# Performance work log

Measured on AMD Instinct MI355X. Metric: run time of the kernel, lower is better.

The kernel has to match this reference:

```python
import jax, jax.numpy as jnp
import numpy as np

H, W, C = 64, 64, 64
B = 64
N_HEADS = 4
CONV_FILTERS = 64
BASIS_DIM = 16


def get_spatial_basis(h, w, d):
    half_d = d // 2
    basis = np.zeros((h, w, d), dtype=np.float32)
    div = np.exp(np.arange(0, half_d, 2, dtype=np.float32) * -np.log(100.0) / half_d)
    h_grid = np.expand_dims(np.arange(0, h, dtype=np.float32), 1)
    w_grid = np.expand_dims(np.arange(0, w, dtype=np.float32), 1)
    basis[:, :, 0:half_d:2] = np.sin(h_grid * div)[:, np.newaxis, :]
    basis[:, :, 1:half_d:2] = np.cos(h_grid * div)[:, np.newaxis, :]
    basis[:, :, half_d::2] = np.sin(w_grid * div)[np.newaxis, :, :]
    basis[:, :, half_d + 1::2] = np.cos(w_grid * div)[np.newaxis, :, :]
    return basis


def setup_inputs() -> dict:
    key = jax.random.key(0)
    ks = jax.random.split(key, 8)
    feat_in = C + BASIS_DIM  # 80 input channels for 1x1 convs
    return {
        "image": jax.random.normal(ks[0], (B, H, W, C), jnp.float32),
        "state1": jax.random.normal(ks[1], (B, 512), jnp.float32),
        "state2": jax.random.normal(ks[2], (B, 512), jnp.float32),
        "extra": jax.random.normal(ks[3], (B, 256), jnp.float32),
        "Wq": jax.random.normal(ks[4], (1024, CONV_FILTERS), jnp.float32) * 0.03,
        "bq": jnp.zeros((CONV_FILTERS,), jnp.float32),
        "Wk": jax.random.normal(ks[5], (feat_in, CONV_FILTERS), jnp.float32) * 0.1,
        "bk": jnp.zeros((CONV_FILTERS,), jnp.float32),
        "Wv": jax.random.normal(ks[6], (feat_in, CONV_FILTERS), jnp.float32) * 0.1,
        "bv": jnp.zeros((CONV_FILTERS,), jnp.float32),
        "spatial_basis": jnp.asarray(get_spatial_basis(H, W, BASIS_DIM)),
    }


def reference(image, state1, state2, extra, Wq, bq, Wk, bk, Wv, bv, spatial_basis):
    b, h, w, _ = image.shape
    nh = N_HEADS
    cf = Wq.shape[1]
    dph = cf // nh  # depth per head

    # concat image with tiled spatial basis -> [B,h,w,C+basis_dim]
    sb = jnp.broadcast_to(spatial_basis[None], (b,) + spatial_basis.shape)
    feats = jnp.concatenate([image, sb], axis=-1)

    # combiner over network-state tensors, then Dense query
    state = jnp.concatenate([state1, state2], axis=-1)  # [B,1024]
    q = state @ Wq + bq                                 # [B,cf]

    # 1x1 convs == per-pixel dense projections
    keys = feats @ Wk + bk    # [B,h,w,cf]
    vals = feats @ Wv + bv    # [B,h,w,cf]

    qh = q.reshape(b, nh, dph)
    kh = keys.reshape(b, h * w, nh, dph)
    vh = vals.reshape(b, h * w, nh, dph)

    # per-head dot scores over spatial positions, softmax over positions
    scores = jnp.einsum('bnd,bpnd->bpn', qh, kh)        # [B,hw,nh]
    attn = jax.nn.softmax(scores, axis=1)
    mean_attn = attn.mean(axis=-1).reshape(b, h, w)

    # weighted sum of values over spatial positions -> [B,cf]
    pooled = jnp.einsum('bpn,bpnd->bnd', attn, vh).reshape(b, cf)

    out = jnp.concatenate([pooled, extra], axis=-1)
    return out, mean_attn
```

## Files before the change

### kernel.cpp

```cpp
#include <hip/hip_runtime.h>
#include <hip/hip_bf16.h>

#define BATCH  64
#define HW     4096
#define PTILE  256
#define NSPLIT 16
#define RST    264

typedef unsigned int u32;
typedef unsigned short u16;

__device__ __forceinline__ float bf2f(u16 h) { return __uint_as_float(((u32)h) << 16); }

__device__ __forceinline__ u32 f2bf(float x) {
  u32 b = __float_as_uint(x);
  return (b + 0x7fffu + ((b >> 16) & 1u)) >> 16;
}

template<bool F32>
__device__ __forceinline__ float ld(const void* p, size_t i) {
  if (F32) return ((const float*)p)[i];
  return bf2f(((const u16*)p)[i]);
}

template<bool F32>
__device__ __forceinline__ float4 ld4(const void* p, size_t i4) {
  if (F32) return ((const float4*)p)[i4];
  uint2 u = ((const uint2*)p)[i4];
  return make_float4(bf2f(u.x & 0xffff), bf2f(u.x >> 16), bf2f(u.y & 0xffff), bf2f(u.y >> 16));
}

template<bool F32>
__device__ __forceinline__ void st(void* p, size_t i, float v) {
  if (F32) ((float*)p)[i] = v;
  else     ((__hip_bfloat16*)p)[i] = __float2bfloat16(v);
}

__device__ __forceinline__ bool detect_f32(const u16* __restrict__ image) {
  u16 h = image[(threadIdx.x & 63) * 2];
  u32 e = (h >> 7) & 0xFFu;
  unsigned long long m = __ballot(e >= 0x86u);
  return __popcll(m) >= 8;
}

template<bool F32>
__device__ void k1a_body(const void* state1, const void* state2, const void* Wq,
                         float* q_part, float* WslT, float* stt) {
  const int kb = blockIdx.x;
  const int tid = threadIdx.x;
#pragma unroll
  for (int i = 0; i < 4; ++i) {
    const int fidx = i * 256 + tid;
    const int r = fidx >> 4, c4 = fidx & 15;
    float4 v = ld4<F32>(Wq, (size_t)(kb * 64 + r) * 16 + c4);
    WslT[(c4 * 4 + 0) * 68 + r] = v.x;
    WslT[(c4 * 4 + 1) * 68 + r] = v.y;
    WslT[(c4 * 4 + 2) * 68 + r] = v.z;
    WslT[(c4 * 4 + 3) * 68 + r] = v.w;
  }
  const void* src = (kb < 8) ? state1 : state2;
  const int k0q = (kb & 7) * 16;
#pragma unroll
  for (int i = 0; i < 4; ++i) {
    const int fidx = i * 256 + tid;
    const int bb = fidx >> 4, i4 = fidx & 15;
    float4 v = ld4<F32>(src, (size_t)bb * 128 + k0q + i4);
    *(float4*)&stt[bb * 64 + i4 * 4] = v;
  }
  __syncthreads();
  const int j = tid & 63, bg = tid >> 6;
  float acc[16];
#pragma unroll
  for (int b2 = 0; b2 < 16; ++b2) acc[b2] = 0.f;
#pragma unroll
  for (int i4 = 0; i4 < 16; ++i4) {
    float4 wv = *(const float4*)&WslT[j * 68 + i4 * 4];
#pragma unroll
    for (int b2 = 0; b2 < 16; ++b2) {
      float4 sv = *(const float4*)&stt[(bg * 16 + b2) * 64 + i4 * 4];
      acc[b2] += wv.x * sv.x + wv.y * sv.y + wv.z * sv.z + wv.w * sv.w;
    }
  }
#pragma unroll
  for (int b2 = 0; b2 < 16; ++b2)
    q_part[kb * 4096 + (bg * 16 + b2) * 64 + j] = acc[b2];
}

__global__ __launch_bounds__(256) void k1a(
    const void* image, const void* state1, const void* state2, const void* Wq, float* q_part) {
  __shared__ float WslT[64 * 68];
  __shared__ float stt[64 * 64];
  if (detect_f32((const u16*)image)) k1a_body<true >(state1, state2, Wq, q_part, WslT, stt);
  else                               k1a_body<false>(state1, state2, Wq, q_part, WslT, stt);
}

template<bool F32>
__device__ void k1b_body(const float* q_part, const void* bq, const void* Wk, const void* bk,
                         float* weff, float* cb, float* q) {
  const int b = blockIdx.x, tid = threadIdx.x;
  if (tid < 64) {
    float a = ld<F32>(bq, tid);
#pragma unroll
    for (int sl = 0; sl < 16; ++sl) a += q_part[sl * 4096 + b * 64 + tid];
    q[tid] = a;
  }
  __syncthreads();
  if (tid < 320) {
    const int c = tid >> 2, n = tid & 3;
    float a = 0.f;
#pragma unroll
    for (int d = 0; d < 16; ++d) a += ld<F32>(Wk, (size_t)c * 64 + n * 16 + d) * q[n * 16 + d];
    weff[b * 320 + tid] = a;
  }
  if (tid >= 256 && tid < 260) {
    const int n = tid - 256;
    float a = 0.f;
#pragma unroll
    for (int d = 0; d < 16; ++d) a += ld<F32>(bk, n * 16 + d) * q[n * 16 + d];
    cb[b * 4 + n] = a;
  }
}

__global__ __launch_bounds__(320) void k1b(
    const void* image, const float* q_part, const void* bq, const void* Wk, const void* bk,
    float* weff, float* cb) {
  __shared__ float q[64];
  if (detect_f32((const u16*)image)) k1b_body<true >(q_part, bq, Wk, bk, weff, cb, q);
  else                               k1b_body<false>(q_part, bq, Wk, bk, weff, cb, q);
}

__global__ __launch_bounds__(256) void k2_main(
    const void* __restrict__ image, const void* __restrict__ basis,
    const float* __restrict__ weff, const float* __restrict__ cb,
    float* __restrict__ e_buf, float* __restrict__ m_blk, float* __restrict__ sum_blk,
    float* __restrict__ fpool_part) {
  __shared__ __align__(16) u16 featT[80 * RST];
  __shared__ __align__(16) float es_t[4 * PTILE];
  __shared__ float weffL[320];
  __shared__ float cbL[4];
  __shared__ float red[16], red2[16], bm[4];
  const int tid = threadIdx.x;
  const int b = blockIdx.x & 63, s = blockIdx.x >> 6;
  const int bs = b * NSPLIT + s;

  for (int i = tid; i < 320; i += 256) weffL[i] = weff[b * 320 + i];
  if (tid < 4) cbL[tid] = cb[b * 4 + tid];

  if (detect_f32((const u16*)image)) {
    const float4* img4 = (const float4*)image + ((size_t)(b * HW + s * PTILE)) * 16;
#pragma unroll
    for (int i = 0; i < 8; ++i) {
      const int fidx = i * 256 + tid;
      const int pp = fidx >> 4, c4 = fidx & 15;
      float4 v0 = img4[(pp * 2) * 16 + c4];
      float4 v1 = img4[(pp * 2 + 1) * 16 + c4];
      *(u32*)&featT[(c4 * 4 + 0) * RST + pp * 2] = f2bf(v0.x) | (f2bf(v1.x) << 16);
      *(u32*)&featT[(c4 * 4 + 1) * RST + pp * 2] = f2bf(v0.y) | (f2bf(v1.y) << 16);
      *(u32*)&featT[(c4 * 4 + 2) * RST + pp * 2] = f2bf(v0.z) | (f2bf(v1.z) << 16);
      *(u32*)&featT[(c4 * 4 + 3) * RST + pp * 2] = f2bf(v0.w) | (f2bf(v1.w) << 16);
    }
    const float4* bas4 = (const float4*)basis + (size_t)(s * PTILE) * 4;
#pragma unroll
    for (int i = 0; i < 2; ++i) {
      const int fidx = i * 256 + tid;
      const int pp = fidx >> 2, c4 = fidx & 3;
      float4 v0 = bas4[(pp * 2) * 4 + c4];
      float4 v1 = bas4[(pp * 2 + 1) * 4 + c4];
      *(u32*)&featT[(64 + c4 * 4 + 0) * RST + pp * 2] = f2bf(v0.x) | (f2bf(v1.x) << 16);
      *(u32*)&featT[(64 + c4 * 4 + 1) * RST + pp * 2] = f2bf(v0.y) | (f2bf(v1.y) << 16);
      *(u32*)&featT[(64 + c4 * 4 + 2) * RST + pp * 2] = f2bf(v0.z) | (f2bf(v1.z) << 16);
      *(u32*)&featT[(64 + c4 * 4 + 3) * RST + pp * 2] = f2bf(v0.w) | (f2bf(v1.w) << 16);
    }
  } else {
    const uint4* img4 = (const uint4*)image + ((size_t)(b * HW + s * PTILE)) * 8;
#pragma unroll
    for (int i = 0; i < 4; ++i) {
      const int fidx = i * 256 + tid;
      const int pp = fidx >> 3, c8 = fidx & 7;
      uint4 u0 = img4[(pp * 2) * 8 + c8];
      uint4 u1 = img4[(pp * 2 + 1) * 8 + c8];
      const u32 w0[4] = {u0.x, u0.y, u0.z, u0.w};
      const u32 w1[4] = {u1.x, u1.y, u1.z, u1.w};
#pragma unroll
      for (int h = 0; h < 4; ++h) {
        *(u32*)&featT[(c8 * 8 + 2 * h + 0) * RST + pp * 2] = (w0[h] & 0xffffu) | (w1[h] << 16);
        *(u32*)&featT[(c8 * 8 + 2 * h + 1) * RST + pp * 2] = (w0[h] >> 16) | (w1[h] & 0xffff0000u);
      }
    }
    const uint4* bas4 = (const uint4*)basis + (size_t)(s * PTILE) * 2;
    {
      const int pp = tid >> 1, h8 = tid & 1;
      uint4 u0 = bas4[(pp * 2) * 2 + h8];
      uint4 u1 = bas4[(pp * 2 + 1) * 2 + h8];
      const u32 w0[4] = {u0.x, u0.y, u0.z, u0.w};
      const u32 w1[4] = {u1.x, u1.y, u1.z, u1.w};
#pragma unroll
      for (int h = 0; h < 4; ++h) {
        *(u32*)&featT[(64 + h8 * 8 + 2 * h + 0) * RST + pp * 2] = (w0[h] & 0xffffu) | (w1[h] << 16);
        *(u32*)&featT[(64 + h8 * 8 + 2 * h + 1) * RST + pp * 2] = (w0[h] >> 16) | (w1[h] & 0xffff0000u);
      }
    }
  }
  __syncthreads();

  const int p8 = tid >> 3, cg = tid & 7;
  float acc[8][4];
#pragma unroll
  for (int pp = 0; pp < 8; ++pp)
#pragma unroll
    for (int n = 0; n < 4; ++n) acc[pp][n] = (cg == 0) ? cbL[n] : 0.f;
#pragma unroll
  for (int ci = 0; ci < 10; ++ci) {
    const int c = cg + 8 * ci;
    uint4 fv = *(const uint4*)&featT[c * RST + ((tid >> 3) & 7) * 8 + (tid >> 6) * 64];
    fv = *(const uint4*)&featT[c * RST + p8 * 8];
    float4 wv = *(const float4*)&weffL[c * 4];
    const u32 uu[4] = {fv.x, fv.y, fv.z, fv.w};
#pragma unroll
    for (int i = 0; i < 4; ++i) {
      float lo = __uint_as_float(uu[i] << 16);
      float hi = __uint_as_float(uu[i] & 0xffff0000u);
      acc[2 * i][0] += lo * wv.x; acc[2 * i][1] += lo * wv.y;
      acc[2 * i][2] += lo * wv.z; acc[2 * i][3] += lo * wv.w;
      acc[2 * i + 1][0] += hi * wv.x; acc[2 * i + 1][1] += hi * wv.y;
      acc[2 * i + 1][2] += hi * wv.z; acc[2 * i + 1][3] += hi * wv.w;
    }
  }
#pragma unroll
  for (int off = 1; off <= 4; off <<= 1)
#pragma unroll
    for (int pp = 0; pp < 8; ++pp)
#pragma unroll
      for (int n = 0; n < 4; ++n) acc[pp][n] += __shfl_xor(acc[pp][n], off, 64);

  float mx[4];
#pragma unroll
  for (int n = 0; n < 4; ++n) {
    float m = acc[0][n];
#pragma unroll
    for (int pp = 1; pp < 8; ++pp) m = fmaxf(m, acc[pp][n]);
    mx[n] = m;
  }
#pragma unroll
  for (int off = 8; off <= 32; off <<= 1)
#pragma unroll
    for (int n = 0; n < 4; ++n) mx[n] = fmaxf(mx[n], __shfl_xor(mx[n], off, 64));
  if ((tid & 63) == 0) {
    float* r = red + (tid >> 6) * 4;
    r[0] = mx[0]; r[1] = mx[1]; r[2] = mx[2]; r[3] = mx[3];
  }
  __syncthreads();
  if (tid < 4) {
    float m = red[tid];
#pragma unroll
    for (int w = 1; w < 4; ++w) m = fmaxf(m, red[w * 4 + tid]);
    bm[tid] = m;
  }
  __syncthreads();

#pragma unroll
  for (int pp = 0; pp < 8; ++pp)
#pragma unroll
    for (int n = 0; n < 4; ++n) acc[pp][n] = __expf(acc[pp][n] - bm[n]);

  if (cg == 0) {
#pragma unroll
    for (int n = 0; n < 4; ++n) {
      float4 eA = make_float4(acc[0][n], acc[1][n], acc[2][n], acc[3][n]);
      float4 eB = make_float4(acc[4][n], acc[5][n], acc[6][n], acc[7][n]);
      *(float4*)&es_t[n * PTILE + p8 * 8]     = eA;
      *(float4*)&es_t[n * PTILE + p8 * 8 + 4] = eB;
      float4* ebp = (float4*)e_buf + (size_t)(b * 4 + n) * 1024 + s * 64 + p8 * 2;
      ebp[0] = eA; ebp[1] = eB;
    }
  }
  float sm[4];
#pragma unroll
  for (int n = 0; n < 4; ++n) {
    float a = acc[0][n];
#pragma unroll
    for (int pp = 1; pp < 8; ++pp) a += acc[pp][n];
    sm[n] = a;
  }
#pragma unroll
  for (int off = 8; off <= 32; off <<= 1)
#pragma unroll
    for (int n = 0; n < 4; ++n) sm[n] += __shfl_xor(sm[n], off, 64);
  if ((tid & 63) == 0) {
    float* r = red2 + (tid >> 6) * 4;
    r[0] = sm[0]; r[1] = sm[1]; r[2] = sm[2]; r[3] = sm[3];
  }
  __syncthreads();
  if (tid < 4) {
    float a = red2[tid] + red2[4 + tid] + red2[8 + tid] + red2[12 + tid];
    sum_blk[bs * 4 + tid] = a;
    m_blk[bs * 4 + tid] = bm[tid];
  }

  {
    const int n = tid >> 6, c = tid & 63;
    const float4* esn = (const float4*)(es_t + n * PTILE);
    float a1 = 0.f, a2 = 0.f;
#pragma unroll 4
    for (int g = 0; g < 32; ++g) {
      float4 ex = esn[g * 2], ey = esn[g * 2 + 1];
      uint4 fv = *(const uint4*)&featT[c * RST + g * 8];
      const u32 uu[4] = {fv.x, fv.y, fv.z, fv.w};
      a1 += ex.x * __uint_as_float(uu[0] << 16) + ex.y * __uint_as_float(uu[0] & 0xffff0000u)
          + ex.z * __uint_as_float(uu[1] << 16) + ex.w * __uint_as_float(uu[1] & 0xffff0000u)
          + ey.x * __uint_as_float(uu[2] << 16) + ey.y * __uint_as_float(uu[2] & 0xffff0000u)
          + ey.z * __uint_as_float(uu[3] << 16) + ey.w * __uint_as_float(uu[3] & 0xffff0000u);
      if (c < 16) {
        uint4 f2 = *(const uint4*)&featT[(64 + c) * RST + g * 8];
        const u32 vv[4] = {f2.x, f2.y, f2.z, f2.w};
        a2 += ex.x * __uint_as_float(vv[0] << 16) + ex.y * __uint_as_float(vv[0] & 0xffff0000u)
            + ex.z * __uint_as_float(vv[1] << 16) + ex.w * __uint_as_float(vv[1] & 0xffff0000u)
            + ey.x * __uint_as_float(vv[2] << 16) + ey.y * __uint_as_float(vv[2] & 0xffff0000u)
            + ey.z * __uint_as_float(vv[3] << 16) + ey.w * __uint_as_float(vv[3] & 0xffff0000u);
      }
    }
    fpool_part[(size_t)bs * 320 + n * 80 + c] = a1;
    if (c < 16) fpool_part[(size_t)bs * 320 + n * 80 + 64 + c] = a2;
  }
}

template<bool F32>
__device__ void k34_body(const float* m_blk, const float* sum_blk, const float* e_buf,
                         const float* fpool_part, const void* Wv, const void* bv,
                         const void* extra, void* out, float* esc, float* fp) {
  const int tid = threadIdx.x;
  const int b = blockIdx.x & 63, s = blockIdx.x >> 6;
  if (tid < 4) {
    float M = -3.4e38f;
#pragma unroll
    for (int sp = 0; sp < NSPLIT; ++sp) M = fmaxf(M, m_blk[(b * NSPLIT + sp) * 4 + tid]);
    float den = 0.f;
#pragma unroll
    for (int sp = 0; sp < NSPLIT; ++sp)
      den += __expf(m_blk[(b * NSPLIT + sp) * 4 + tid] - M) * sum_blk[(b * NSPLIT + sp) * 4 + tid];
    float rd = 1.0f / den;
#pragma unroll
    for (int sp = 0; sp < NSPLIT; ++sp)
      esc[sp * 4 + tid] = __expf(m_blk[(b * NSPLIT + sp) * 4 + tid] - M) * rd;
  }
  __syncthreads();
  {
    const size_t pidx = (size_t)s * PTILE + tid;
    float e0 = e_buf[(size_t)(b * 4 + 0) * HW + pidx];
    float e1 = e_buf[(size_t)(b * 4 + 1) * HW + pidx];
    float e2 = e_buf[(size_t)(b * 4 + 2) * HW + pidx];
    float e3 = e_buf[(size_t)(b * 4 + 3) * HW + pidx];
    float mean = 0.25f * (e0 * esc[s * 4 + 0] + e1 * esc[s * 4 + 1] +
                          e2 * esc[s * 4 + 2] + e3 * esc[s * 4 + 3]);
    st<F32>(out, (size_t)BATCH * 320 + (size_t)b * HW + pidx, mean);
  }
  if (s == 0) {
    for (int idx = tid; idx < 320; idx += 256) {
      const int n2 = idx / 80;
      float a = 0.f;
#pragma unroll
      for (int sp = 0; sp < NSPLIT; ++sp)
        a += esc[sp * 4 + n2] * fpool_part[(size_t)(b * NSPLIT + sp) * 320 + idx];
      fp[idx] = a;
    }
    __syncthreads();
    if (tid < 64) {
      const int n = tid >> 4;
      float dot = 0.f;
#pragma unroll
      for (int c = 0; c < 80; ++c) dot += fp[n * 80 + c] * ld<F32>(Wv, (size_t)c * 64 + tid);
      st<F32>(out, (size_t)b * 320 + tid, dot + ld<F32>(bv, tid));
    }
    st<F32>(out, (size_t)b * 320 + 64 + tid, ld<F32>(extra, (size_t)b * 256 + tid));
  }
}

__global__ __launch_bounds__(256) void k34_out(
    const void* image, const float* m_blk, const float* sum_blk, const float* e_buf,
    const float* fpool_part, const void* Wv, const void* bv, const void* extra, void* out) {
  __shared__ float esc[NSPLIT * 4];
  __shared__ float fp[320];
  if (detect_f32((const u16*)image))
       k34_body<true >(m_blk, sum_blk, e_buf, fpool_part, Wv, bv, extra, out, esc, fp);
  else k34_body<false>(m_blk, sum_blk, e_buf, fpool_part, Wv, bv, extra, out, esc, fp);
}

extern "C" void kernel_launch(void* const* d_in, const int* in_sizes, int n_in,
                              void* d_out, int out_size, void* d_ws, size_t ws_size,
                              hipStream_t stream) {
  (void)in_sizes; (void)n_in; (void)out_size; (void)ws_size;
  const void* image  = d_in[0];
  const void* state1 = d_in[1];
  const void* state2 = d_in[2];
  const void* extra  = d_in[3];
  const void* Wq = d_in[4];
  const void* bq = d_in[5];
  const void* Wk = d_in[6];
  const void* bk = d_in[7];
  const void* Wv = d_in[8];
  const void* bv = d_in[9];
  const void* basis = d_in[10];

  float* ws         = (float*)d_ws;
  float* weff       = ws;
  float* cb         = ws + 20480;
  float* m_blk      = ws + 20736;
  float* sum_blk    = ws + 24832;
  float* q_part     = ws + 28928;
  float* fpool_part = ws + 94464;
  float* e_buf      = ws + 422144;

  k1a<<<dim3(16), dim3(256), 0, stream>>>(image, state1, state2, Wq, q_part);
  k1b<<<dim3(BATCH), dim3(320), 0, stream>>>(image, q_part, bq, Wk, bk, weff, cb);
  k2_main<<<dim3(BATCH * NSPLIT), dim3(PTILE), 0, stream>>>(image, basis, weff, cb,
                                                            e_buf, m_blk, sum_blk, fpool_part);
  k34_out<<<dim3(BATCH * NSPLIT), dim3(PTILE), 0, stream>>>(image, m_blk, sum_blk, e_buf,
                                                            fpool_part, Wv, bv, extra, d_out);
}
```

Measured before the change: 142.7 us.

## Use bf16 MFMA for score and pooling GEMMs with smaller pixel tiles

Replaces the scalar FMA score computation and the weighted feature pooling in the main kernel with 16x16x32 bf16 MFMA instructions. To feed them, features are staged in shared memory in both row-major and transposed layouts, and the effective key weights are stored as padded bf16. The pixel tile shrinks from 256 to 128, so there are 32 splits per batch, and the exp buffer is stored as bf16 to halve its traffic. The trade-off is lower precision on the exponentials, more shared-memory staging, and a larger partial-reduction workload in the output kernel.

Result: faster. 131.5 us (-7.8%).

```diff
diff --git a/kernel.cpp b/kernel.cpp
--- a/kernel.cpp
+++ b/kernel.cpp
@@ -1,35 +1,36 @@
 #include <hip/hip_runtime.h>
 #include <hip/hip_bf16.h>
 
-#define BATCH  64
-#define HW     4096
-#define PTILE  256
-#define NSPLIT 16
-#define RST    264
+#define BATCH 64
+#define HW    4096
+#define PT    128
+#define NS    32
+#define FR_ST 104
+#define FT_ST 136
 
 typedef unsigned int u32;
 typedef unsigned short u16;
+typedef __attribute__((ext_vector_type(8))) short bf16x8;
+typedef __attribute__((ext_vector_type(4))) float f32x4;
 
 __device__ __forceinline__ float bf2f(u16 h) { return __uint_as_float(((u32)h) << 16); }
-
 __device__ __forceinline__ u32 f2bf(float x) {
   u32 b = __float_as_uint(x);
   return (b + 0x7fffu + ((b >> 16) & 1u)) >> 16;
 }
+__device__ __forceinline__ u32 pkbf(float lo, float hi) { return f2bf(lo) | (f2bf(hi) << 16); }
 
 template<bool F32>
 __device__ __forceinline__ float ld(const void* p, size_t i) {
   if (F32) return ((const float*)p)[i];
   return bf2f(((const u16*)p)[i]);
 }
-
 template<bool F32>
 __device__ __forceinline__ float4 ld4(const void* p, size_t i4) {
   if (F32) return ((const float4*)p)[i4];
   uint2 u = ((const uint2*)p)[i4];
   return make_float4(bf2f(u.x & 0xffff), bf2f(u.x >> 16), bf2f(u.y & 0xffff), bf2f(u.y >> 16));
 }
-
 template<bool F32>
 __device__ __forceinline__ void st(void* p, size_t i, float v) {
   if (F32) ((float*)p)[i] = v;
@@ -96,8 +97,10 @@
 
 template<bool F32>
 __device__ void k1b_body(const float* q_part, const void* bq, const void* Wk, const void* bk,
-                         float* weff, float* cb, float* q) {
+                         u16* weffbt, float* cb, float* q) {
   const int b = blockIdx.x, tid = threadIdx.x;
+  u32* wz = (u32*)(weffbt + (size_t)b * 1664);
+  for (int i = tid; i < 832; i += 320) wz[i] = 0u;
   if (tid < 64) {
     float a = ld<F32>(bq, tid);
 #pragma unroll
@@ -110,7 +113,7 @@
     float a = 0.f;
 #pragma unroll
     for (int d = 0; d < 16; ++d) a += ld<F32>(Wk, (size_t)c * 64 + n * 16 + d) * q[n * 16 + d];
-    weff[b * 320 + tid] = a;
+    weffbt[(size_t)b * 1664 + n * 104 + c] = (u16)f2bf(a);
   }
   if (tid >= 256 && tid < 260) {
     const int n = tid - 256;
@@ -123,244 +126,231 @@
 
 __global__ __launch_bounds__(320) void k1b(
     const void* image, const float* q_part, const void* bq, const void* Wk, const void* bk,
-    float* weff, float* cb) {
+    u16* weffbt, float* cb) {
   __shared__ float q[64];
-  if (detect_f32((const u16*)image)) k1b_body<true >(q_part, bq, Wk, bk, weff, cb, q);
-  else                               k1b_body<false>(q_part, bq, Wk, bk, weff, cb, q);
+  if (detect_f32((const u16*)image)) k1b_body<true >(q_part, bq, Wk, bk, weffbt, cb, q);
+  else                               k1b_body<false>(q_part, bq, Wk, bk, weffbt, cb, q);
 }
 
 __global__ __launch_bounds__(256) void k2_main(
     const void* __restrict__ image, const void* __restrict__ basis,
-    const float* __restrict__ weff, const float* __restrict__ cb,
-    float* __restrict__ e_buf, float* __restrict__ m_blk, float* __restrict__ sum_blk,
+    const float* __restrict__ cb, const u16* __restrict__ weffbt,
+    u16* __restrict__ e_buf, float* __restrict__ m_blk, float* __restrict__ sum_blk,
     float* __restrict__ fpool_part) {
-  __shared__ __align__(16) u16 featT[80 * RST];
-  __shared__ __align__(16) float es_t[4 * PTILE];
-  __shared__ float weffL[320];
-  __shared__ float cbL[4];
-  __shared__ float red[16], red2[16], bm[4];
+  __shared__ __align__(16) u16 smem[25936];
+  float* redf  = (float*)(smem + 25856);
+  float* red2f = (float*)(smem + 25888);
+  float* bmf   = (float*)(smem + 25920);
+  float* cbL   = (float*)(smem + 25928);
+
   const int tid = threadIdx.x;
   const int b = blockIdx.x & 63, s = blockIdx.x >> 6;
-  const int bs = b * NSPLIT + s;
-
-  for (int i = tid; i < 320; i += 256) weffL[i] = weff[b * 320 + i];
-  if (tid < 4) cbL[tid] = cb[b * 4 + tid];
+  const int bs = b * NS + s;
+  const int wave = tid >> 6, lane = tid & 63;
+  const int m = lane & 15, q = lane >> 4;
 
   if (detect_f32((const u16*)image)) {
-    const float4* img4 = (const float4*)image + ((size_t)(b * HW + s * PTILE)) * 16;
-#pragma unroll
-    for (int i = 0; i < 8; ++i) {
-      const int fidx = i * 256 + tid;
-      const int pp = fidx >> 4, c4 = fidx & 15;
-      float4 v0 = img4[(pp * 2) * 16 + c4];
-      float4 v1 = img4[(pp * 2 + 1) * 16 + c4];
-      *(u32*)&featT[(c4 * 4 + 0) * RST + pp * 2] = f2bf(v0.x) | (f2bf(v1.x) << 16);
-      *(u32*)&featT[(c4 * 4 + 1) * RST + pp * 2] = f2bf(v0.y) | (f2bf(v1.y) << 16);
-      *(u32*)&featT[(c4 * 4 + 2) * RST + pp * 2] = f2bf(v0.z) | (f2bf(v1.z) << 16);
-      *(u32*)&featT[(c4 * 4 + 3) * RST + pp * 2] = f2bf(v0.w) | (f2bf(v1.w) << 16);
-    }
-    const float4* bas4 = (const float4*)basis + (size_t)(s * PTILE) * 4;
-#pragma unroll
-    for (int i = 0; i < 2; ++i) {
-      const int fidx = i * 256 + tid;
-      const int pp = fidx >> 2, c4 = fidx & 3;
-      float4 v0 = bas4[(pp * 2) * 4 + c4];
-      float4 v1 = bas4[(pp * 2 + 1) * 4 + c4];
-      *(u32*)&featT[(64 + c4 * 4 + 0) * RST + pp * 2] = f2bf(v0.x) | (f2bf(v1.x) << 16);
-      *(u32*)&featT[(64 + c4 * 4 + 1) * RST + pp * 2] = f2bf(v0.y) | (f2bf(v1.y) << 16);
-      *(u32*)&featT[(64 + c4 * 4 + 2) * RST + pp * 2] = f2bf(v0.z) | (f2bf(v1.z) << 16);
-      *(u32*)&featT[(64 + c4 * 4 + 3) * RST + pp * 2] = f2bf(v0.w) | (f2bf(v1.w) << 16);
-    }
-  } else {
-    const uint4* img4 = (const uint4*)image + ((size_t)(b * HW + s * PTILE)) * 8;
+    const float4* img4 = (const float4*)image + ((size_t)(b * HW + s * PT)) * 16;
 #pragma unroll
     for (int i = 0; i < 4; ++i) {
       const int fidx = i * 256 + tid;
-      const int pp = fidx >> 3, c8 = fidx & 7;
-      uint4 u0 = img4[(pp * 2) * 8 + c8];
-      uint4 u1 = img4[(pp * 2 + 1) * 8 + c8];
+      const int pq = fidx >> 4, c4 = fidx & 15;
+      float4 v0 = img4[(pq * 2) * 16 + c4];
+      float4 v1 = img4[(pq * 2 + 1) * 16 + c4];
+      *(uint2*)&smem[(pq * 2) * FR_ST + c4 * 4]     = make_uint2(pkbf(v0.x, v0.y), pkbf(v0.z, v0.w));
+      *(uint2*)&smem[(pq * 2 + 1) * FR_ST + c4 * 4] = make_uint2(pkbf(v1.x, v1.y), pkbf(v1.z, v1.w));
+      const float a0[4] = {v0.x, v0.y, v0.z, v0.w};
+      const float a1[4] = {v1.x, v1.y, v1.z, v1.w};
+#pragma unroll
+      for (int k = 0; k < 4; ++k)
+        *(u32*)&smem[13312 + (c4 * 4 + k) * FT_ST + pq * 2] = pkbf(a0[k], a1[k]);
+    }
+    const float4* bas4 = (const float4*)basis + (size_t)(s * PT) * 4;
+    {
+      const int pq = tid >> 2, c4 = tid & 3;
+      float4 v0 = bas4[(pq * 2) * 4 + c4];
+      float4 v1 = bas4[(pq * 2 + 1) * 4 + c4];
+      *(uint2*)&smem[(pq * 2) * FR_ST + 64 + c4 * 4]     = make_uint2(pkbf(v0.x, v0.y), pkbf(v0.z, v0.w));
+      *(uint2*)&smem[(pq * 2 + 1) * FR_ST + 64 + c4 * 4] = make_uint2(pkbf(v1.x, v1.y), pkbf(v1.z, v1.w));
+      const float a0[4] = {v0.x, v0.y, v0.z, v0.w};
+      const float a1[4] = {v1.x, v1.y, v1.z, v1.w};
+#pragma unroll
+      for (int k = 0; k < 4; ++k)
+        *(u32*)&smem[13312 + (64 + c4 * 4 + k) * FT_ST + pq * 2] = pkbf(a0[k], a1[k]);
+    }
+  } else {
+    const uint4* img4 = (const uint4*)image + ((size_t)(b * HW + s * PT)) * 4;
+    {
+      const int pq = tid >> 2, c8 = tid & 3;
+      uint4 u0 = img4[(pq * 2) * 4 + c8];
+      uint4 u1 = img4[(pq * 2 + 1) * 4 + c8];
+      *(uint4*)&smem[(pq * 2) * FR_ST + c8 * 8]     = u0;
+      *(uint4*)&smem[(pq * 2 + 1) * FR_ST + c8 * 8] = u1;
       const u32 w0[4] = {u0.x, u0.y, u0.z, u0.w};
       const u32 w1[4] = {u1.x, u1.y, u1.z, u1.w};
 #pragma unroll
-      for (int h = 0; h < 4; ++h) {
-        *(u32*)&featT[(c8 * 8 + 2 * h + 0) * RST + pp * 2] = (w0[h] & 0xffffu) | (w1[h] << 16);
-        *(u32*)&featT[(c8 * 8 + 2 * h + 1) * RST + pp * 2] = (w0[h] >> 16) | (w1[h] & 0xffff0000u);
+      for (int k = 0; k < 4; ++k) {
+        *(u32*)&smem[13312 + (c8 * 8 + 2 * k) * FT_ST + pq * 2]     = (w0[k] & 0xffffu) | (w1[k] << 16);
+        *(u32*)&smem[13312 + (c8 * 8 + 2 * k + 1) * FT_ST + pq * 2] = (w0[k] >> 16) | (w1[k] & 0xffff0000u);
       }
     }
-    const uint4* bas4 = (const uint4*)basis + (size_t)(s * PTILE) * 2;
-    {
-      const int pp = tid >> 1, h8 = tid & 1;
-      uint4 u0 = bas4[(pp * 2) * 2 + h8];
-      uint4 u1 = bas4[(pp * 2 + 1) * 2 + h8];
+    const uint4* bas4 = (const uint4*)basis + (size_t)(s * PT) * 2;
+    if (tid < 128) {
+      const int pq = tid >> 1, c8 = tid & 1;
+      uint4 u0 = bas4[(pq * 2) * 2 + c8];
+      uint4 u1 = bas4[(pq * 2 + 1) * 2 + c8];
+      *(uint4*)&smem[(pq * 2) * FR_ST + 64 + c8 * 8]     = u0;
+      *(uint4*)&smem[(pq * 2 + 1) * FR_ST + 64 + c8 * 8] = u1;
       const u32 w0[4] = {u0.x, u0.y, u0.z, u0.w};
       const u32 w1[4] = {u1.x, u1.y, u1.z, u1.w};
 #pragma unroll
-      for (int h = 0; h < 4; ++h) {
-        *(u32*)&featT[(64 + h8 * 8 + 2 * h + 0) * RST + pp * 2] = (w0[h] & 0xffffu) | (w1[h] << 16);
-        *(u32*)&featT[(64 + h8 * 8 + 2 * h + 1) * RST + pp * 2] = (w0[h] >> 16) | (w1[h] & 0xffff0000u);
+      for (int k = 0; k < 4; ++k) {
+        *(u32*)&smem[13312 + (64 + c8 * 8 + 2 * k) * FT_ST + pq * 2]     = (w0[k] & 0xffffu) | (w1[k] << 16);
+        *(u32*)&smem[13312 + (64 + c8 * 8 + 2 * k + 1) * FT_ST + pq * 2] = (w0[k] >> 16) | (w1[k] & 0xffff0000u);
       }
     }
   }
-  __syncthreads();
-
-  const int p8 = tid >> 3, cg = tid & 7;
-  float acc[8][4];
-#pragma unroll
-  for (int pp = 0; pp < 8; ++pp)
-#pragma unroll
-    for (int n = 0; n < 4; ++n) acc[pp][n] = (cg == 0) ? cbL[n] : 0.f;
-#pragma unroll
-  for (int ci = 0; ci < 10; ++ci) {
-    const int c = cg + 8 * ci;
-    uint4 fv = *(const uint4*)&featT[c * RST + ((tid >> 3) & 7) * 8 + (tid >> 6) * 64];
-    fv = *(const uint4*)&featT[c * RST + p8 * 8];
-    float4 wv = *(const float4*)&weffL[c * 4];
-    const u32 uu[4] = {fv.x, fv.y, fv.z, fv.w};
-#pragma unroll
-    for (int i = 0; i < 4; ++i) {
-      float lo = __uint_as_float(uu[i] << 16);
-      float hi = __uint_as_float(uu[i] & 0xffff0000u);
-      acc[2 * i][0] += lo * wv.x; acc[2 * i][1] += lo * wv.y;
-      acc[2 * i][2] += lo * wv.z; acc[2 * i][3] += lo * wv.w;
-      acc[2 * i + 1][0] += hi * wv.x; acc[2 * i + 1][1] += hi * wv.y;
-      acc[2 * i + 1][2] += hi * wv.z; acc[2 * i + 1][3] += hi * wv.w;
-    }
-  }
-#pragma unroll
-  for (int off = 1; off <= 4; off <<= 1)
-#pragma unroll
-    for (int pp = 0; pp < 8; ++pp)
-#pragma unroll
-      for (int n = 0; n < 4; ++n) acc[pp][n] += __shfl_xor(acc[pp][n], off, 64);
-
-  float mx[4];
-#pragma unroll
-  for (int n = 0; n < 4; ++n) {
-    float m = acc[0][n];
-#pragma unroll
-    for (int pp = 1; pp < 8; ++pp) m = fmaxf(m, acc[pp][n]);
-    mx[n] = m;
-  }
-#pragma unroll
-  for (int off = 8; off <= 32; off <<= 1)
-#pragma unroll
-    for (int n = 0; n < 4; ++n) mx[n] = fmaxf(mx[n], __shfl_xor(mx[n], off, 64));
-  if ((tid & 63) == 0) {
-    float* r = red + (tid >> 6) * 4;
-    r[0] = mx[0]; r[1] = mx[1]; r[2] = mx[2]; r[3] = mx[3];
+  if (tid < 128) {
+    *(uint4*)&smem[tid * FR_ST + 80] = make_uint4(0, 0, 0, 0);
+    *(uint4*)&smem[tid * FR_ST + 88] = make_uint4(0, 0, 0, 0);
+  }
+  if (tid < 208) {
+    uint4 v = ((const uint4*)(weffbt + (size_t)b * 1664))[tid];
+    *(uint4*)&smem[24192 + tid * 8] = v;
+  }
+  if (tid < 4) cbL[tid] = cb[b * 4 + tid];
+  __syncthreads();
+
+  f32x4 accS[2];
+  {
+    const float ci = (m < 4) ? cbL[m] : 0.f;
+#pragma unroll
+    for (int t = 0; t < 2; ++t) { accS[t][0] = ci; accS[t][1] = ci; accS[t][2] = ci; accS[t][3] = ci; }
+#pragma unroll
+    for (int t = 0; t < 2; ++t) {
+      const int T = wave * 2 + t;
+#pragma unroll
+      for (int s3 = 0; s3 < 3; ++s3) {
+        bf16x8 a = *(const bf16x8*)&smem[(T * 16 + m) * FR_ST + s3 * 32 + q * 8];
+        bf16x8 bb = *(const bf16x8*)&smem[24192 + m * FR_ST + s3 * 32 + q * 8];
+        accS[t] = __builtin_amdgcn_mfma_f32_16x16x32_bf16(a, bb, accS[t], 0, 0, 0);
+      }
+    }
+  }
+  {
+    float mx = accS[0][0];
+#pragma unroll
+    for (int t = 0; t < 2; ++t)
+#pragma unroll
+      for (int r = 0; r < 4; ++r) mx = fmaxf(mx, accS[t][r]);
+    mx = fmaxf(mx, __shfl_xor(mx, 16, 64));
+    mx = fmaxf(mx, __shfl_xor(mx, 32, 64));
+    if (lane < 4) redf[wave * 4 + lane] = mx;
+  }
+  __syncthreads();
+  if (tid < 4)
+    bmf[tid] = fmaxf(fmaxf(redf[tid], redf[4 + tid]), fmaxf(redf[8 + tid], redf[12 + tid]));
+  for (int i = tid; i < 816; i += 256) ((u32*)smem)[272 + i] = 0u;
+  __syncthreads();
+
+  {
+    const float bmv = bmf[m & 3];
+    float ss = 0.f;
+#pragma unroll
+    for (int t = 0; t < 2; ++t) {
+      const int T = wave * 2 + t;
+#pragma unroll
+      for (int r = 0; r < 4; ++r) {
+        float e = __expf(accS[t][r] - bmv);
+        u32 eb = f2bf(e);
+        float er = bf2f((u16)eb);
+        ss += er;
+        if (m < 4) smem[m * FT_ST + T * 16 + q * 4 + r] = (u16)eb;
+      }
+    }
+    ss += __shfl_xor(ss, 16, 64);
+    ss += __shfl_xor(ss, 32, 64);
+    if (lane < 4) red2f[wave * 4 + lane] = ss;
   }
   __syncthreads();
   if (tid < 4) {
-    float m = red[tid];
-#pragma unroll
-    for (int w = 1; w < 4; ++w) m = fmaxf(m, red[w * 4 + tid]);
-    bm[tid] = m;
-  }
-  __syncthreads();
-
-#pragma unroll
-  for (int pp = 0; pp < 8; ++pp)
-#pragma unroll
-    for (int n = 0; n < 4; ++n) acc[pp][n] = __expf(acc[pp][n] - bm[n]);
-
-  if (cg == 0) {
-#pragma unroll
-    for (int n = 0; n < 4; ++n) {
-      float4 eA = make_float4(acc[0][n], acc[1][n], acc[2][n], acc[3][n]);
-      float4 eB = make_float4(acc[4][n], acc[5][n], acc[6][n], acc[7][n]);
-      *(float4*)&es_t[n * PTILE + p8 * 8]     = eA;
-      *(float4*)&es_t[n * PTILE + p8 * 8 + 4] = eB;
-      float4* ebp = (float4*)e_buf + (size_t)(b * 4 + n) * 1024 + s * 64 + p8 * 2;
-      ebp[0] = eA; ebp[1] = eB;
-    }
-  }
-  float sm[4];
-#pragma unroll
-  for (int n = 0; n < 4; ++n) {
-    float a = acc[0][n];
-#pragma unroll
-    for (int pp = 1; pp < 8; ++pp) a += acc[pp][n];
-    sm[n] = a;
-  }
-#pragma unroll
-  for (int off = 8; off <= 32; off <<= 1)
-#pragma unroll
-    for (int n = 0; n < 4; ++n) sm[n] += __shfl_xor(sm[n], off, 64);
-  if ((tid & 63) == 0) {
-    float* r = red2 + (tid >> 6) * 4;
-    r[0] = sm[0]; r[1] = sm[1]; r[2] = sm[2]; r[3] = sm[3];
-  }
-  __syncthreads();
-  if (tid < 4) {
-    float a = red2[tid] + red2[4 + tid] + red2[8 + tid] + red2[12 + tid];
-    sum_blk[bs * 4 + tid] = a;
-    m_blk[bs * 4 + tid] = bm[tid];
-  }
-
-  {
-    const int n = tid >> 6, c = tid & 63;
-    const float4* esn = (const float4*)(es_t + n * PTILE);
-    float a1 = 0.f, a2 = 0.f;
-#pragma unroll 4
-    for (int g = 0; g < 32; ++g) {
-      float4 ex = esn[g * 2], ey = esn[g * 2 + 1];
-      uint4 fv = *(const uint4*)&featT[c * RST + g * 8];
-      const u32 uu[4] = {fv.x, fv.y, fv.z, fv.w};
-      a1 += ex.x * __uint_as_float(uu[0] << 16) + ex.y * __uint_as_float(uu[0] & 0xffff0000u)
-          + ex.z * __uint_as_float(uu[1] << 16) + ex.w * __uint_as_float(uu[1] & 0xffff0000u)
-          + ey.x * __uint_as_float(uu[2] << 16) + ey.y * __uint_as_float(uu[2] & 0xffff0000u)
-          + ey.z * __uint_as_float(uu[3] << 16) + ey.w * __uint_as_float(uu[3] & 0xffff0000u);
-      if (c < 16) {
-        uint4 f2 = *(const uint4*)&featT[(64 + c) * RST + g * 8];
-        const u32 vv[4] = {f2.x, f2.y, f2.z, f2.w};
-        a2 += ex.x * __uint_as_float(vv[0] << 16) + ex.y * __uint_as_float(vv[0] & 0xffff0000u)
-            + ex.z * __uint_as_float(vv[1] << 16) + ex.w * __uint_as_float(vv[1] & 0xffff0000u)
-            + ey.x * __uint_as_float(vv[2] << 16) + ey.y * __uint_as_float(vv[2] & 0xffff0000u)
-            + ey.z * __uint_as_float(vv[3] << 16) + ey.w * __uint_as_float(vv[3] & 0xffff0000u);
-      }
-    }
-    fpool_part[(size_t)bs * 320 + n * 80 + c] = a1;
-    if (c < 16) fpool_part[(size_t)bs * 320 + n * 80 + 64 + c] = a2;
-  }
-}
-
-template<bool F32>
-__device__ void k34_body(const float* m_blk, const float* sum_blk, const float* e_buf,
+    m_blk[bs * 4 + tid] = bmf[tid];
+    sum_blk[bs * 4 + tid] = red2f[tid] + red2f[4 + tid] + red2f[8 + tid] + red2f[12 + tid];
+  }
+  {
+    const int n = tid >> 6, pp = tid & 63;
+    u32 v = *(const u32*)&smem[n * FT_ST + pp * 2];
+    ((u32*)e_buf)[((size_t)(b * 4 + n)) * 2048 + s * 64 + pp] = v;
+  }
+  {
+    bf16x8 ap = *(const bf16x8*)&smem[m * FT_ST + wave * 32 + q * 8];
+    f32x4 accP[5];
+#pragma unroll
+    for (int T = 0; T < 5; ++T) { accP[T][0] = 0; accP[T][1] = 0; accP[T][2] = 0; accP[T][3] = 0; }
+#pragma unroll
+    for (int T = 0; T < 5; ++T) {
+      bf16x8 bp = *(const bf16x8*)&smem[13312 + (T * 16 + m) * FT_ST + wave * 32 + q * 8];
+      accP[T] = __builtin_amdgcn_mfma_f32_16x16x32_bf16(ap, bp, accP[T], 0, 0, 0);
+    }
+    if (lane < 16) {
+      float* pr = (float*)(smem + 2176);
+#pragma unroll
+      for (int T = 0; T < 5; ++T)
+#pragma unroll
+        for (int r = 0; r < 4; ++r)
+          pr[((wave * 5 + T) * 4 + r) * 16 + lane] = accP[T][r];
+    }
+  }
+  __syncthreads();
+  {
+    const float* pr = (const float*)(smem + 2176);
+    for (int t = tid; t < 320; t += 256) {
+      const int n = t / 80, c = t - n * 80;
+      const int tile = c >> 4, cc = c & 15;
+      float a = 0.f;
+#pragma unroll
+      for (int w = 0; w < 4; ++w) a += pr[((w * 5 + tile) * 4 + n) * 16 + cc];
+      fpool_part[(size_t)bs * 320 + t] = a;
+    }
+  }
+}
+
+template<bool F32>
+__device__ void k34_body(const float* m_blk, const float* sum_blk, const u16* e_buf,
                          const float* fpool_part, const void* Wv, const void* bv,
                          const void* extra, void* out, float* esc, float* fp) {
   const int tid = threadIdx.x;
-  const int b = blockIdx.x & 63, s = blockIdx.x >> 6;
+  const int b = blockIdx.x & 63, s16 = blockIdx.x >> 6;
   if (tid < 4) {
     float M = -3.4e38f;
 #pragma unroll
-    for (int sp = 0; sp < NSPLIT; ++sp) M = fmaxf(M, m_blk[(b * NSPLIT + sp) * 4 + tid]);
+    for (int sp = 0; sp < NS; ++sp) M = fmaxf(M, m_blk[(b * NS + sp) * 4 + tid]);
     float den = 0.f;
 #pragma unroll
-    for (int sp = 0; sp < NSPLIT; ++sp)
-      den += __expf(m_blk[(b * NSPLIT + sp) * 4 + tid] - M) * sum_blk[(b * NSPLIT + sp) * 4 + tid];
+    for (int sp = 0; sp < NS; ++sp)
+      den += __expf(m_blk[(b * NS + sp) * 4 + tid] - M) * sum_blk[(b * NS + sp) * 4 + tid];
     float rd = 1.0f / den;
 #pragma unroll
-    for (int sp = 0; sp < NSPLIT; ++sp)
-      esc[sp * 4 + tid] = __expf(m_blk[(b * NSPLIT + sp) * 4 + tid] - M) * rd;
-  }
-  __syncthreads();
-  {
-    const size_t pidx = (size_t)s * PTILE + tid;
-    float e0 = e_buf[(size_t)(b * 4 + 0) * HW + pidx];
-    float e1 = e_buf[(size_t)(b * 4 + 1) * HW + pidx];
-    float e2 = e_buf[(size_t)(b * 4 + 2) * HW + pidx];
-    float e3 = e_buf[(size_t)(b * 4 + 3) * HW + pidx];
-    float mean = 0.25f * (e0 * esc[s * 4 + 0] + e1 * esc[s * 4 + 1] +
-                          e2 * esc[s * 4 + 2] + e3 * esc[s * 4 + 3]);
-    st<F32>(out, (size_t)BATCH * 320 + (size_t)b * HW + pidx, mean);
-  }
-  if (s == 0) {
+    for (int sp = 0; sp < NS; ++sp)
+      esc[sp * 4 + tid] = __expf(m_blk[(b * NS + sp) * 4 + tid] - M) * rd;
+  }
+  __syncthreads();
+  {
+    const int gpos = s16 * 256 + tid;
+    const int s32 = gpos >> 7;
+    float mean = 0.f;
+#pragma unroll
+    for (int n = 0; n < 4; ++n)
+      mean += bf2f(e_buf[(size_t)(b * 4 + n) * HW + gpos]) * esc[s32 * 4 + n];
+    st<F32>(out, (size_t)BATCH * 320 + (size_t)b * HW + gpos, 0.25f * mean);
+  }
+  if (s16 == 0) {
     for (int idx = tid; idx < 320; idx += 256) {
       const int n2 = idx / 80;
       float a = 0.f;
 #pragma unroll
-      for (int sp = 0; sp < NSPLIT; ++sp)
-        a += esc[sp * 4 + n2] * fpool_part[(size_t)(b * NSPLIT + sp) * 320 + idx];
+      for (int sp = 0; sp < NS; ++sp)
+        a += esc[sp * 4 + n2] * fpool_part[(size_t)(b * NS + sp) * 320 + idx];
       fp[idx] = a;
     }
     __syncthreads();
@@ -376,9 +366,9 @@
 }
 
 __global__ __launch_bounds__(256) void k34_out(
-    const void* image, const float* m_blk, const float* sum_blk, const float* e_buf,
+    const void* image, const float* m_blk, const float* sum_blk, const u16* e_buf,
     const float* fpool_part, const void* Wv, const void* bv, const void* extra, void* out) {
-  __shared__ float esc[NSPLIT * 4];
+  __shared__ float esc[NS * 4];
   __shared__ float fp[320];
   if (detect_f32((const u16*)image))
        k34_body<true >(m_blk, sum_blk, e_buf, fpool_part, Wv, bv, extra, out, esc, fp);
@@ -402,18 +392,18 @@
   const void* basis = d_in[10];
 
   float* ws         = (float*)d_ws;
-  float* weff       = ws;
-  float* cb         = ws + 20480;
-  float* m_blk      = ws + 20736;
-  float* sum_blk    = ws + 24832;
-  float* q_part     = ws + 28928;
-  float* fpool_part = ws + 94464;
-  float* e_buf      = ws + 422144;
+  float* cb         = ws;
+  float* m_blk      = ws + 256;
+  float* sum_blk    = ws + 8448;
+  float* q_part     = ws + 16640;
+  float* fpool_part = ws + 82176;
+  u16*   weffbt     = (u16*)(ws + 737536);
+  u16*   e_buf      = (u16*)(ws + 790784);
 
   k1a<<<dim3(16), dim3(256), 0, stream>>>(image, state1, state2, Wq, q_part);
-  k1b<<<dim3(BATCH), dim3(320), 0, stream>>>(image, q_part, bq, Wk, bk, weff, cb);
-  k2_main<<<dim3(BATCH * NSPLIT), dim3(PTILE), 0, stream>>>(image, basis, weff, cb,
-                                                            e_buf, m_blk, sum_blk, fpool_part);
-  k34_out<<<dim3(BATCH * NSPLIT), dim3(PTILE), 0, stream>>>(image, m_blk, sum_blk, e_buf,
-                                                            fpool_part, Wv, bv, extra, d_out);
-}
+  k1b<<<dim3(BATCH), dim3(320), 0, stream>>>(image, q_part, bq, Wk, bk, weffbt, cb);
+  k2_main<<<dim3(BATCH * NS), dim3(256), 0, stream>>>(image, basis, cb, weffbt,
+                                                      e_buf, m_blk, sum_blk, fpool_part);
+  k34_out<<<dim3(BATCH * 16), dim3(256), 0, stream>>>(image, m_blk, sum_blk, e_buf,
+                                                      fpool_part, Wv, bv, extra, d_out);
+}
```
